# Kernel optimization log

Measured on AMD Instinct MI355X. Metric: run time of the kernel, lower is better.

The kernel has to match this reference:

```python
import jax, jax.numpy as jnp
import numpy as np

NX, NY = 1024, 512
LX, LY = 0.26, 0.12
NU = 1e-4
U_INLET = 0.1
DX = LX / (NX - 1)
DY = LY / (NY - 1)
W_CONT, W_MOM, W_BC = 1.0, 0.1, 1.0


def _pad_x(f):
    # replicate pad along x axis (dim -2)
    return jnp.pad(f, ((0, 0), (0, 0), (1, 1), (0, 0)), mode='edge')


def _pad_y(f):
    return jnp.pad(f, ((0, 0), (0, 0), (0, 0), (1, 1)), mode='edge')


def ddx(f):
    p = _pad_x(f)
    return (p[:, :, 2:, :] - p[:, :, :-2, :]) / (2.0 * DX)


def ddy(f):
    p = _pad_y(f)
    return (p[:, :, :, 2:] - p[:, :, :, :-2]) / (2.0 * DY)


def d2dx2(f):
    p = _pad_x(f)
    return (p[:, :, 2:, :] - 2.0 * f + p[:, :, :-2, :]) / (DX * DX)


def d2dy2(f):
    p = _pad_y(f)
    return (p[:, :, :, 2:] - 2.0 * f + p[:, :, :, :-2]) / (DY * DY)


def masked_mean(x, mask):
    return (x * mask).sum() / jnp.maximum(mask.sum(), 1.0)


def region_masks(x_in):
    r = x_in[:, 1:2].astype(jnp.float32)  # [B,1,NX,NY] region codes
    fluid = (r > 0.5).astype(jnp.float32)
    obstacle = (r < 0.5).astype(jnp.float32)
    wall = ((r > 1.5) & (r < 2.5)).astype(jnp.float32)
    inlet = ((r > 2.5) & (r < 3.5)).astype(jnp.float32)
    outlet = (r > 3.5).astype(jnp.float32)
    noslip = ((obstacle + wall) > 0.5).astype(jnp.float32)
    # interior = fluid with zeroed 1-cell border
    border = jnp.zeros((NX, NY), jnp.float32).at[1:-1, 1:-1].set(1.0)
    interior = fluid * border
    return fluid, interior, noslip, inlet, outlet


def setup_inputs() -> dict:
    key = jax.random.key(0)
    k1, k2 = jax.random.split(key)
    y_hat = jax.random.normal(k1, (16, 3, NX, NY), dtype=jnp.float32)
    x_in = jax.random.randint(k2, (16, 2, NX, NY), 0, 5).astype(jnp.int32)
    return {'y_hat': y_hat, 'x_in': x_in}


def reference(y_hat, x_in):
    ux = y_hat[:, 0:1]
    uy = y_hat[:, 1:2]
    p = y_hat[:, 2:3]
    fluid, interior, noslip, inlet, outlet = region_masks(x_in)

    # continuity
    div = ddx(ux) + ddy(uy)
    l_cont = masked_mean(div ** 2, interior)

    # momentum
    res_x = ux * ddx(ux) + uy * ddy(ux) + ddx(p) - NU * (d2dx2(ux) + d2dy2(ux))
    res_y = ux * ddx(uy) + uy * ddy(uy) + ddy(p) - NU * (d2dx2(uy) + d2dy2(uy))
    l_mom = masked_mean(res_x ** 2, interior) + masked_mean(res_y ** 2, interior)

    # boundary (masked_mean already returns 0 for empty masks via denom clamp)
    l_bc = masked_mean(ux ** 2, noslip) + masked_mean(uy ** 2, noslip)
    l_bc = l_bc + masked_mean((ux - U_INLET) ** 2, inlet) + masked_mean(uy ** 2, inlet)
    l_bc = l_bc + masked_mean(ddx(ux) ** 2, outlet)

    total = W_CONT * l_cont + W_MOM * l_mom + W_BC * l_bc
    return jnp.stack([l_cont, l_mom, l_bc, total])
```

## Files before the change

### kernel.cpp

```cpp
#include <hip/hip_runtime.h>


namespace {
constexpr int NXc  = 1024;
constexpr int NYc  = 512;
constexpr int NXYc = NXc * NYc;
constexpr int NBc  = 16;
constexpr int NTHR = 512;
constexpr int NACC = 10;
constexpr int TR   = 8;
constexpr int NCH  = NXc / TR;
constexpr int NBLK = NBc * NCH;
constexpr int NXCD = 8;
constexpr int QX   = NBLK / NXCD;
}

__global__ __launch_bounds__(NTHR) void pil_main(const float* __restrict__ y,
                                                 const int* __restrict__ xin,
                                                 float* __restrict__ partial) {
  constexpr double DXd = 0.26 / 1023.0;
  constexpr double DYd = 0.12 / 511.0;
  const float INV2DX = (float)(1.0 / (2.0 * DXd));
  const float INV2DY = (float)(1.0 / (2.0 * DYd));
  const float INVDX2 = (float)(1.0 / (DXd * DXd));
  const float INVDY2 = (float)(1.0 / (DYd * DYd));
  constexpr float NU = 1e-4f;
  constexpr float U_INLET = 0.1f;

  __shared__ float lf[3][TR + 2][NYc];

  const int l   = threadIdx.x & 63;
  const int w   = threadIdx.x >> 6;
  const int swz = (blockIdx.x % NXCD) * QX + blockIdx.x / NXCD;
  const int b   = swz >> 7;
  const int i0  = (swz & (NCH - 1)) * TR;

  const float* __restrict__ ux = y + (size_t)b * 3 * NXYc;
  const float* __restrict__ uy = ux + NXYc;
  const float* __restrict__ pp = ux + 2 * NXYc;
  const int*   __restrict__ rp = xin + (size_t)(2 * b + 1) * NXYc;

  for (int c = w; c < 60; c += 8) {
    const int f  = c / 20;
    const int cc = c % 20;
    const int rw = cc >> 1;
    const int h  = cc & 1;
    int gi = i0 - 1 + rw;
    gi = gi < 0 ? 0 : (gi > NXc - 1 ? NXc - 1 : gi);
    const float* base = (f == 0) ? ux : ((f == 1) ? uy : pp);
    const float* g = base + gi * NYc + h * 256 + l * 4;
    float* d = &lf[f][rw][h * 256];
    __builtin_amdgcn_global_load_lds(
        (const __attribute__((address_space(1))) void*)g,
        (__attribute__((address_space(3))) void*)d, 16, 0, 0);
  }

  const int i = i0 + w;
  const int4 R0 = *reinterpret_cast<const int4*>(rp + i * NYc + (l << 2));
  const int4 R1 = *reinterpret_cast<const int4*>(rp + i * NYc + 256 + (l << 2));

  __syncthreads();

  float a[NACC];
#pragma unroll
  for (int k = 0; k < NACC; ++k) a[k] = 0.f;

  const bool irow = (i >= 1) & (i <= NXc - 2);

#pragma unroll
  for (int h = 0; h < 2; ++h) {
    const int j0 = h * 256 + (l << 2);

    const float4 Cx = *reinterpret_cast<const float4*>(&lf[0][w + 1][j0]);
    const float4 Cy = *reinterpret_cast<const float4*>(&lf[1][w + 1][j0]);
    const float4 Cp = *reinterpret_cast<const float4*>(&lf[2][w + 1][j0]);
    const float4 Px = *reinterpret_cast<const float4*>(&lf[0][w][j0]);
    const float4 Py = *reinterpret_cast<const float4*>(&lf[1][w][j0]);
    const float4 Pp = *reinterpret_cast<const float4*>(&lf[2][w][j0]);
    const float4 Nx = *reinterpret_cast<const float4*>(&lf[0][w + 2][j0]);
    const float4 Ny = *reinterpret_cast<const float4*>(&lf[1][w + 2][j0]);
    const float4 Np = *reinterpret_cast<const float4*>(&lf[2][w + 2][j0]);
    const int4   R4 = h ? R1 : R0;

    const int jm = (j0 == 0) ? 0 : j0 - 1;
    const int jp = (j0 + 4 > NYc - 1) ? NYc - 1 : j0 + 4;
    const float lx = lf[0][w + 1][jm], rx = lf[0][w + 1][jp];
    const float ly = lf[1][w + 1][jm], ry = lf[1][w + 1][jp];
    const float lq = lf[2][w + 1][jm], rq = lf[2][w + 1][jp];

    const float cx[6]  = {lx, Cx.x, Cx.y, Cx.z, Cx.w, rx};
    const float cy_[6] = {ly, Cy.x, Cy.y, Cy.z, Cy.w, ry};
    const float cp_[6] = {lq, Cp.x, Cp.y, Cp.z, Cp.w, rq};
    const float pxA[4] = {Px.x, Px.y, Px.z, Px.w};
    const float pyA[4] = {Py.x, Py.y, Py.z, Py.w};
    const float ppA[4] = {Pp.x, Pp.y, Pp.z, Pp.w};
    const float nxA[4] = {Nx.x, Nx.y, Nx.z, Nx.w};
    const float nyA[4] = {Ny.x, Ny.y, Ny.z, Ny.w};
    const float npA[4] = {Np.x, Np.y, Np.z, Np.w};
    const int   rA[4]  = {R4.x, R4.y, R4.z, R4.w};

#pragma unroll
    for (int e = 0; e < 4; ++e) {
      const int   rg   = rA[e];
      const float c_ux = cx[e + 1], c_uy = cy_[e + 1];
      const float uxm = cx[e],      uxp = cx[e + 2];
      const float uym = cy_[e],     uyp = cy_[e + 2];
      const float pm_ = cp_[e],     pq_ = cp_[e + 2];

      const float ddx_ux = (nxA[e] - pxA[e]) * INV2DX;
      const float ddy_ux = (uxp - uxm) * INV2DY;
      const float ddx_uy = (nyA[e] - pyA[e]) * INV2DX;
      const float ddy_uy = (uyp - uym) * INV2DY;

      const int j = j0 + e;
      const bool jedge = (j == 0) | (j == NYc - 1);
      const bool interior = (rg >= 1) & irow & (!jedge);
      if (interior) {
        const float dv    = ddx_ux + ddy_uy;
        const float d2xux = (nxA[e] - 2.f * c_ux + pxA[e]) * INVDX2;
        const float d2yux = (uxp - 2.f * c_ux + uxm) * INVDY2;
        const float d2xuy = (nyA[e] - 2.f * c_uy + pyA[e]) * INVDX2;
        const float d2yuy = (uyp - 2.f * c_uy + uym) * INVDY2;
        const float ddx_p = (npA[e] - ppA[e]) * INV2DX;
        const float ddy_p = (pq_ - pm_) * INV2DY;
        const float rxv = c_ux * ddx_ux + c_uy * ddy_ux + ddx_p - NU * (d2xux + d2yux);
        const float ryv = c_ux * ddx_uy + c_uy * ddy_uy + ddy_p - NU * (d2xuy + d2yuy);
        a[0] += dv * dv;
        a[1] += rxv * rxv;
        a[2] += ryv * ryv;
        a[3] += 1.f;
      }
      if ((rg == 0) | (rg == 2)) {
        a[4] += c_ux * c_ux + c_uy * c_uy;
        a[5] += 1.f;
      }
      if (rg == 3) {
        const float d = c_ux - U_INLET;
        a[6] += d * d + c_uy * c_uy;
        a[7] += 1.f;
      }
      if (rg == 4) {
        a[8] += ddx_ux * ddx_ux;
        a[9] += 1.f;
      }
    }
  }

#pragma unroll
  for (int k = 0; k < NACC; ++k) {
    float v = a[k];
#pragma unroll
    for (int off = 32; off > 0; off >>= 1) v += __shfl_down(v, off, 64);
    a[k] = v;
  }

  __shared__ float sacc[NTHR / 64][NACC];
  if (l == 0) {
#pragma unroll
    for (int k = 0; k < NACC; ++k) sacc[w][k] = a[k];
  }
  __syncthreads();
  if (threadIdx.x < NACC) {
    float s = 0.f;
#pragma unroll
    for (int ww = 0; ww < NTHR / 64; ++ww) s += sacc[ww][threadIdx.x];
    partial[threadIdx.x * NBLK + blockIdx.x] = s;
  }
}

__global__ __launch_bounds__(256) void pil_finalize(const float* __restrict__ partial,
                                                    float* __restrict__ out) {
  __shared__ double sw[NACC][4];
  const int t = threadIdx.x;
  const int lane = t & 63, wave = t >> 6;
#pragma unroll
  for (int k = 0; k < NACC; ++k) {
    double v = 0.0;
    const float4* p4 = reinterpret_cast<const float4*>(partial + (size_t)k * NBLK);
    for (int bb = t; bb < NBLK / 4; bb += 256) {
      const float4 q = p4[bb];
      v += (double)q.x + (double)q.y + (double)q.z + (double)q.w;
    }
#pragma unroll
    for (int off = 32; off > 0; off >>= 1) v += __shfl_down(v, off, 64);
    if (lane == 0) sw[k][wave] = v;
  }
  __syncthreads();
  if (t == 0) {
    double acc[NACC];
#pragma unroll
    for (int k = 0; k < NACC; ++k) {
      double s = 0.0;
#pragma unroll
      for (int ww = 0; ww < 4; ++ww) s += sw[k][ww];
      acc[k] = s;
    }
    const double l_cont = acc[0] / fmax(acc[3], 1.0);
    const double l_mom  = (acc[1] + acc[2]) / fmax(acc[3], 1.0);
    const double l_bc   = acc[4] / fmax(acc[5], 1.0)
                        + acc[6] / fmax(acc[7], 1.0)
                        + acc[8] / fmax(acc[9], 1.0);
    const double total  = 1.0 * l_cont + 0.1 * l_mom + 1.0 * l_bc;
    out[0] = (float)l_cont;
    out[1] = (float)l_mom;
    out[2] = (float)l_bc;
    out[3] = (float)total;
  }
}

extern "C" void kernel_launch(void* const* d_in, const int* in_sizes, int n_in,
                              void* d_out, int out_size, void* d_ws, size_t ws_size,
                              hipStream_t stream) {
  const float* y   = (const float*)d_in[0];
  const int*   xin = (const int*)d_in[1];
  float* partial   = (float*)d_ws;

  pil_main<<<NBLK, NTHR, 0, stream>>>(y, xin, partial);
  pil_finalize<<<1, 256, 0, stream>>>(partial, (float*)d_out);
}
```

Measured before the change: 47.16 us.

## Make blocks persistent over eight row tiles with double-buffered async LDS staging

Each block now processes eight consecutive 8-row tiles instead of one, giving 256 blocks in total. The next tile's halo rows are staged into a second LDS buffer with global_load_lds while the current tile is computed, using manual vmcnt waits and barriers. This amortizes launch cost and overlaps memory with compute. In exchange it needs 120 KB of dynamic LDS per block, which cuts occupancy to one block per CU, and it relies on hand-counted vmcnt values. The finalize kernel now reads one partial per thread since there are only 256 partials.

```diff
diff --git a/kernel.cpp b/kernel.cpp
--- a/kernel.cpp
+++ b/kernel.cpp
@@ -9,15 +9,18 @@
 constexpr int NTHR = 512;
 constexpr int NACC = 10;
 constexpr int TR   = 8;
-constexpr int NCH  = NXc / TR;
-constexpr int NBLK = NBc * NCH;
+constexpr int TPB  = 8;
+constexpr int NBLK = NBc * NXc / (TR * TPB);
 constexpr int NXCD = 8;
 constexpr int QX   = NBLK / NXCD;
+constexpr int BUFE = 3 * (TR + 2) * NYc;
 }
 
 __global__ __launch_bounds__(NTHR) void pil_main(const float* __restrict__ y,
                                                  const int* __restrict__ xin,
                                                  float* __restrict__ partial) {
+  extern __shared__ float lds[];
+
   constexpr double DXd = 0.26 / 1023.0;
   constexpr double DYd = 0.12 / 511.0;
   const float INV2DX = (float)(1.0 / (2.0 * DXd));
@@ -27,123 +30,152 @@
   constexpr float NU = 1e-4f;
   constexpr float U_INLET = 0.1f;
 
-  __shared__ float lf[3][TR + 2][NYc];
-
   const int l   = threadIdx.x & 63;
   const int w   = threadIdx.x >> 6;
   const int swz = (blockIdx.x % NXCD) * QX + blockIdx.x / NXCD;
-  const int b   = swz >> 7;
-  const int i0  = (swz & (NCH - 1)) * TR;
+  const int b   = swz >> 4;
+  const int sub = swz & 15;
+  const int bi0 = sub * (TR * TPB);
 
   const float* __restrict__ ux = y + (size_t)b * 3 * NXYc;
   const float* __restrict__ uy = ux + NXYc;
   const float* __restrict__ pp = ux + 2 * NXYc;
   const int*   __restrict__ rp = xin + (size_t)(2 * b + 1) * NXYc;
 
-  for (int c = w; c < 60; c += 8) {
-    const int f  = c / 20;
-    const int cc = c % 20;
-    const int rw = cc >> 1;
-    const int h  = cc & 1;
-    int gi = i0 - 1 + rw;
-    gi = gi < 0 ? 0 : (gi > NXc - 1 ? NXc - 1 : gi);
-    const float* base = (f == 0) ? ux : ((f == 1) ? uy : pp);
-    const float* g = base + gi * NYc + h * 256 + l * 4;
-    float* d = &lf[f][rw][h * 256];
-    __builtin_amdgcn_global_load_lds(
-        (const __attribute__((address_space(1))) void*)g,
-        (__attribute__((address_space(3))) void*)d, 16, 0, 0);
-  }
-
-  const int i = i0 + w;
-  const int4 R0 = *reinterpret_cast<const int4*>(rp + i * NYc + (l << 2));
-  const int4 R1 = *reinterpret_cast<const int4*>(rp + i * NYc + 256 + (l << 2));
-
-  __syncthreads();
+  auto stage = [&](int t, int q) {
+    const int ti0 = bi0 + t * TR;
+#pragma unroll
+    for (int k = 0; k < 8; ++k) {
+      const int c = k * 8 + w;
+      if (c < 60) {
+        const int f  = c / 20;
+        const int cc = c % 20;
+        const int rw = cc >> 1;
+        const int h  = cc & 1;
+        int gi = ti0 - 1 + rw;
+        gi = gi < 0 ? 0 : (gi > NXc - 1 ? NXc - 1 : gi);
+        const float* base = (f == 0) ? ux : ((f == 1) ? uy : pp);
+        const float* g = base + gi * NYc + h * 256 + l * 4;
+        float* d = lds + q * BUFE + f * ((TR + 2) * NYc) + rw * NYc + h * 256;
+        __builtin_amdgcn_global_load_lds(
+            (const __attribute__((address_space(1))) void*)g,
+            (__attribute__((address_space(3))) void*)d, 16, 0, 0);
+      }
+    }
+  };
 
   float a[NACC];
 #pragma unroll
   for (int k = 0; k < NACC; ++k) a[k] = 0.f;
 
-  const bool irow = (i >= 1) & (i <= NXc - 2);
-
-#pragma unroll
-  for (int h = 0; h < 2; ++h) {
-    const int j0 = h * 256 + (l << 2);
-
-    const float4 Cx = *reinterpret_cast<const float4*>(&lf[0][w + 1][j0]);
-    const float4 Cy = *reinterpret_cast<const float4*>(&lf[1][w + 1][j0]);
-    const float4 Cp = *reinterpret_cast<const float4*>(&lf[2][w + 1][j0]);
-    const float4 Px = *reinterpret_cast<const float4*>(&lf[0][w][j0]);
-    const float4 Py = *reinterpret_cast<const float4*>(&lf[1][w][j0]);
-    const float4 Pp = *reinterpret_cast<const float4*>(&lf[2][w][j0]);
-    const float4 Nx = *reinterpret_cast<const float4*>(&lf[0][w + 2][j0]);
-    const float4 Ny = *reinterpret_cast<const float4*>(&lf[1][w + 2][j0]);
-    const float4 Np = *reinterpret_cast<const float4*>(&lf[2][w + 2][j0]);
-    const int4   R4 = h ? R1 : R0;
-
-    const int jm = (j0 == 0) ? 0 : j0 - 1;
-    const int jp = (j0 + 4 > NYc - 1) ? NYc - 1 : j0 + 4;
-    const float lx = lf[0][w + 1][jm], rx = lf[0][w + 1][jp];
-    const float ly = lf[1][w + 1][jm], ry = lf[1][w + 1][jp];
-    const float lq = lf[2][w + 1][jm], rq = lf[2][w + 1][jp];
-
-    const float cx[6]  = {lx, Cx.x, Cx.y, Cx.z, Cx.w, rx};
-    const float cy_[6] = {ly, Cy.x, Cy.y, Cy.z, Cy.w, ry};
-    const float cp_[6] = {lq, Cp.x, Cp.y, Cp.z, Cp.w, rq};
-    const float pxA[4] = {Px.x, Px.y, Px.z, Px.w};
-    const float pyA[4] = {Py.x, Py.y, Py.z, Py.w};
-    const float ppA[4] = {Pp.x, Pp.y, Pp.z, Pp.w};
-    const float nxA[4] = {Nx.x, Nx.y, Nx.z, Nx.w};
-    const float nyA[4] = {Ny.x, Ny.y, Ny.z, Ny.w};
-    const float npA[4] = {Np.x, Np.y, Np.z, Np.w};
-    const int   rA[4]  = {R4.x, R4.y, R4.z, R4.w};
-
-#pragma unroll
-    for (int e = 0; e < 4; ++e) {
-      const int   rg   = rA[e];
-      const float c_ux = cx[e + 1], c_uy = cy_[e + 1];
-      const float uxm = cx[e],      uxp = cx[e + 2];
-      const float uym = cy_[e],     uyp = cy_[e + 2];
-      const float pm_ = cp_[e],     pq_ = cp_[e + 2];
-
-      const float ddx_ux = (nxA[e] - pxA[e]) * INV2DX;
-      const float ddy_ux = (uxp - uxm) * INV2DY;
-      const float ddx_uy = (nyA[e] - pyA[e]) * INV2DX;
-      const float ddy_uy = (uyp - uym) * INV2DY;
-
-      const int j = j0 + e;
-      const bool jedge = (j == 0) | (j == NYc - 1);
-      const bool interior = (rg >= 1) & irow & (!jedge);
-      if (interior) {
-        const float dv    = ddx_ux + ddy_uy;
-        const float d2xux = (nxA[e] - 2.f * c_ux + pxA[e]) * INVDX2;
-        const float d2yux = (uxp - 2.f * c_ux + uxm) * INVDY2;
-        const float d2xuy = (nyA[e] - 2.f * c_uy + pyA[e]) * INVDX2;
-        const float d2yuy = (uyp - 2.f * c_uy + uym) * INVDY2;
-        const float ddx_p = (npA[e] - ppA[e]) * INV2DX;
-        const float ddy_p = (pq_ - pm_) * INV2DY;
-        const float rxv = c_ux * ddx_ux + c_uy * ddy_ux + ddx_p - NU * (d2xux + d2yux);
-        const float ryv = c_ux * ddx_uy + c_uy * ddy_uy + ddy_p - NU * (d2xuy + d2yuy);
-        a[0] += dv * dv;
-        a[1] += rxv * rxv;
-        a[2] += ryv * ryv;
-        a[3] += 1.f;
+  stage(0, 0);
+
+#pragma unroll 2
+  for (int t = 0; t < TPB; ++t) {
+    const int q = t & 1;
+    const int i = bi0 + t * TR + w;
+
+    const int4 R0 = *reinterpret_cast<const int4*>(rp + i * NYc + (l << 2));
+    const int4 R1 = *reinterpret_cast<const int4*>(rp + i * NYc + 256 + (l << 2));
+    asm volatile("" ::: "memory");
+
+    if (t + 1 < TPB) {
+      stage(t + 1, q ^ 1);
+      if (w < 4) asm volatile("s_waitcnt vmcnt(8)" ::: "memory");
+      else       asm volatile("s_waitcnt vmcnt(7)" ::: "memory");
+    } else {
+      asm volatile("s_waitcnt vmcnt(0)" ::: "memory");
+    }
+    __builtin_amdgcn_s_barrier();
+    asm volatile("" ::: "memory");
+
+    const float* Lf = lds + q * BUFE;
+#define LF(f, row, col) Lf[(f) * ((TR + 2) * NYc) + (row) * NYc + (col)]
+
+    const bool irow = (i >= 1) & (i <= NXc - 2);
+
+#pragma unroll
+    for (int h = 0; h < 2; ++h) {
+      const int j0 = h * 256 + (l << 2);
+
+      const float4 Cx = *reinterpret_cast<const float4*>(&LF(0, w + 1, j0));
+      const float4 Cy = *reinterpret_cast<const float4*>(&LF(1, w + 1, j0));
+      const float4 Cp = *reinterpret_cast<const float4*>(&LF(2, w + 1, j0));
+      const float4 Px = *reinterpret_cast<const float4*>(&LF(0, w, j0));
+      const float4 Py = *reinterpret_cast<const float4*>(&LF(1, w, j0));
+      const float4 Pp = *reinterpret_cast<const float4*>(&LF(2, w, j0));
+      const float4 Nx = *reinterpret_cast<const float4*>(&LF(0, w + 2, j0));
+      const float4 Ny = *reinterpret_cast<const float4*>(&LF(1, w + 2, j0));
+      const float4 Np = *reinterpret_cast<const float4*>(&LF(2, w + 2, j0));
+      const int4   R4 = h ? R1 : R0;
+
+      const int jm = (j0 == 0) ? 0 : j0 - 1;
+      const int jp = (j0 + 4 > NYc - 1) ? NYc - 1 : j0 + 4;
+      const float lx = LF(0, w + 1, jm), rx = LF(0, w + 1, jp);
+      const float ly = LF(1, w + 1, jm), ry = LF(1, w + 1, jp);
+      const float lq = LF(2, w + 1, jm), rq = LF(2, w + 1, jp);
+
+      const float cx[6]  = {lx, Cx.x, Cx.y, Cx.z, Cx.w, rx};
+      const float cy_[6] = {ly, Cy.x, Cy.y, Cy.z, Cy.w, ry};
+      const float cp_[6] = {lq, Cp.x, Cp.y, Cp.z, Cp.w, rq};
+      const float pxA[4] = {Px.x, Px.y, Px.z, Px.w};
+      const float pyA[4] = {Py.x, Py.y, Py.z, Py.w};
+      const float ppA[4] = {Pp.x, Pp.y, Pp.z, Pp.w};
+      const float nxA[4] = {Nx.x, Nx.y, Nx.z, Nx.w};
+      const float nyA[4] = {Ny.x, Ny.y, Ny.z, Ny.w};
+      const float npA[4] = {Np.x, Np.y, Np.z, Np.w};
+      const int   rA[4]  = {R4.x, R4.y, R4.z, R4.w};
+
+#pragma unroll
+      for (int e = 0; e < 4; ++e) {
+        const int   rg   = rA[e];
+        const float c_ux = cx[e + 1], c_uy = cy_[e + 1];
+        const float uxm = cx[e],      uxp = cx[e + 2];
+        const float uym = cy_[e],     uyp = cy_[e + 2];
+        const float pm_ = cp_[e],     pq_ = cp_[e + 2];
+
+        const float ddx_ux = (nxA[e] - pxA[e]) * INV2DX;
+        const float ddy_ux = (uxp - uxm) * INV2DY;
+        const float ddx_uy = (nyA[e] - pyA[e]) * INV2DX;
+        const float ddy_uy = (uyp - uym) * INV2DY;
+
+        const int j = j0 + e;
+        const bool jedge = (j == 0) | (j == NYc - 1);
+        const bool interior = (rg >= 1) & irow & (!jedge);
+        if (interior) {
+          const float dv    = ddx_ux + ddy_uy;
+          const float d2xux = (nxA[e] - 2.f * c_ux + pxA[e]) * INVDX2;
+          const float d2yux = (uxp - 2.f * c_ux + uxm) * INVDY2;
+          const float d2xuy = (nyA[e] - 2.f * c_uy + pyA[e]) * INVDX2;
+          const float d2yuy = (uyp - 2.f * c_uy + uym) * INVDY2;
+          const float ddx_p = (npA[e] - ppA[e]) * INV2DX;
+          const float ddy_p = (pq_ - pm_) * INV2DY;
+          const float rxv = c_ux * ddx_ux + c_uy * ddy_ux + ddx_p - NU * (d2xux + d2yux);
+          const float ryv = c_ux * ddx_uy + c_uy * ddy_uy + ddy_p - NU * (d2xuy + d2yuy);
+          a[0] += dv * dv;
+          a[1] += rxv * rxv;
+          a[2] += ryv * ryv;
+          a[3] += 1.f;
+        }
+        if ((rg == 0) | (rg == 2)) {
+          a[4] += c_ux * c_ux + c_uy * c_uy;
+          a[5] += 1.f;
+        }
+        if (rg == 3) {
+          const float d = c_ux - U_INLET;
+          a[6] += d * d + c_uy * c_uy;
+          a[7] += 1.f;
+        }
+        if (rg == 4) {
+          a[8] += ddx_ux * ddx_ux;
+          a[9] += 1.f;
+        }
       }
-      if ((rg == 0) | (rg == 2)) {
-        a[4] += c_ux * c_ux + c_uy * c_uy;
-        a[5] += 1.f;
-      }
-      if (rg == 3) {
-        const float d = c_ux - U_INLET;
-        a[6] += d * d + c_uy * c_uy;
-        a[7] += 1.f;
-      }
-      if (rg == 4) {
-        a[8] += ddx_ux * ddx_ux;
-        a[9] += 1.f;
-      }
-    }
+    }
+#undef LF
+
+    asm volatile("" ::: "memory");
+    __builtin_amdgcn_s_barrier();
   }
 
 #pragma unroll
@@ -154,16 +186,16 @@
     a[k] = v;
   }
 
-  __shared__ float sacc[NTHR / 64][NACC];
+  float* sacc = lds;
   if (l == 0) {
 #pragma unroll
-    for (int k = 0; k < NACC; ++k) sacc[w][k] = a[k];
+    for (int k = 0; k < NACC; ++k) sacc[w * NACC + k] = a[k];
   }
   __syncthreads();
   if (threadIdx.x < NACC) {
     float s = 0.f;
 #pragma unroll
-    for (int ww = 0; ww < NTHR / 64; ++ww) s += sacc[ww][threadIdx.x];
+    for (int ww = 0; ww < NTHR / 64; ++ww) s += sacc[ww * NACC + threadIdx.x];
     partial[threadIdx.x * NBLK + blockIdx.x] = s;
   }
 }
@@ -175,12 +207,7 @@
   const int lane = t & 63, wave = t >> 6;
 #pragma unroll
   for (int k = 0; k < NACC; ++k) {
-    double v = 0.0;
-    const float4* p4 = reinterpret_cast<const float4*>(partial + (size_t)k * NBLK);
-    for (int bb = t; bb < NBLK / 4; bb += 256) {
-      const float4 q = p4[bb];
-      v += (double)q.x + (double)q.y + (double)q.z + (double)q.w;
-    }
+    double v = (double)partial[k * NBLK + t];
 #pragma unroll
     for (int off = 32; off > 0; off >>= 1) v += __shfl_down(v, off, 64);
     if (lane == 0) sw[k][wave] = v;
@@ -215,6 +242,7 @@
   const int*   xin = (const int*)d_in[1];
   float* partial   = (float*)d_ws;
 
-  pil_main<<<NBLK, NTHR, 0, stream>>>(y, xin, partial);
+  const size_t dyn_lds = 2 * (size_t)BUFE * sizeof(float);
+  pil_main<<<NBLK, NTHR, dyn_lds, stream>>>(y, xin, partial);
   pil_finalize<<<1, 256, 0, stream>>>(partial, (float*)d_out);
 }
```

Measured after the change: 88.89 us. +88.5%, slower.

## Halve row tile and block size, give each lane 8 contiguous columns with shuffle halos

Applied to the files above, without the earlier changes.

Blocks shrink from 512 to 256 threads and from 8 to 4 rows, doubling the block count and halving the shared tile. Each lane now handles 8 contiguous columns and gets its left and right neighbours through wavefront shuffles instead of extra scalar LDS reads. The staging loop is fully unrolled at 9 iterations. More blocks mean more halo rows re-read from global memory and more partial sums for the finalize kernel to reduce.

```diff
diff --git a/kernel.cpp b/kernel.cpp
--- a/kernel.cpp
+++ b/kernel.cpp
@@ -6,9 +6,9 @@
 constexpr int NYc  = 512;
 constexpr int NXYc = NXc * NYc;
 constexpr int NBc  = 16;
-constexpr int NTHR = 512;
+constexpr int NTHR = 256;
 constexpr int NACC = 10;
-constexpr int TR   = 8;
+constexpr int TR   = 4;
 constexpr int NCH  = NXc / TR;
 constexpr int NBLK = NBc * NCH;
 constexpr int NXCD = 8;
@@ -32,7 +32,7 @@
   const int l   = threadIdx.x & 63;
   const int w   = threadIdx.x >> 6;
   const int swz = (blockIdx.x % NXCD) * QX + blockIdx.x / NXCD;
-  const int b   = swz >> 7;
+  const int b   = swz >> 8;
   const int i0  = (swz & (NCH - 1)) * TR;
 
   const float* __restrict__ ux = y + (size_t)b * 3 * NXYc;
@@ -40,9 +40,11 @@
   const float* __restrict__ pp = ux + 2 * NXYc;
   const int*   __restrict__ rp = xin + (size_t)(2 * b + 1) * NXYc;
 
-  for (int c = w; c < 60; c += 8) {
-    const int f  = c / 20;
-    const int cc = c % 20;
+#pragma unroll
+  for (int k = 0; k < 9; ++k) {
+    const int c  = k * 4 + w;
+    const int f  = c / 12;
+    const int cc = c % 12;
     const int rw = cc >> 1;
     const int h  = cc & 1;
     int gi = i0 - 1 + rw;
@@ -56,93 +58,100 @@
   }
 
   const int i = i0 + w;
-  const int4 R0 = *reinterpret_cast<const int4*>(rp + i * NYc + (l << 2));
-  const int4 R1 = *reinterpret_cast<const int4*>(rp + i * NYc + 256 + (l << 2));
+  const int jc = l << 3;
+  const int4 R0 = *reinterpret_cast<const int4*>(rp + i * NYc + jc);
+  const int4 R1 = *reinterpret_cast<const int4*>(rp + i * NYc + jc + 4);
 
   __syncthreads();
 
+  const float4 Cxl = *reinterpret_cast<const float4*>(&lf[0][w + 1][jc]);
+  const float4 Cxh = *reinterpret_cast<const float4*>(&lf[0][w + 1][jc + 4]);
+  const float4 Cyl = *reinterpret_cast<const float4*>(&lf[1][w + 1][jc]);
+  const float4 Cyh = *reinterpret_cast<const float4*>(&lf[1][w + 1][jc + 4]);
+  const float4 Cpl = *reinterpret_cast<const float4*>(&lf[2][w + 1][jc]);
+  const float4 Cph = *reinterpret_cast<const float4*>(&lf[2][w + 1][jc + 4]);
+  const float4 Pxl = *reinterpret_cast<const float4*>(&lf[0][w][jc]);
+  const float4 Pxh = *reinterpret_cast<const float4*>(&lf[0][w][jc + 4]);
+  const float4 Pyl = *reinterpret_cast<const float4*>(&lf[1][w][jc]);
+  const float4 Pyh = *reinterpret_cast<const float4*>(&lf[1][w][jc + 4]);
+  const float4 Ppl = *reinterpret_cast<const float4*>(&lf[2][w][jc]);
+  const float4 Pph = *reinterpret_cast<const float4*>(&lf[2][w][jc + 4]);
+  const float4 Nxl = *reinterpret_cast<const float4*>(&lf[0][w + 2][jc]);
+  const float4 Nxh = *reinterpret_cast<const float4*>(&lf[0][w + 2][jc + 4]);
+  const float4 Nyl = *reinterpret_cast<const float4*>(&lf[1][w + 2][jc]);
+  const float4 Nyh = *reinterpret_cast<const float4*>(&lf[1][w + 2][jc + 4]);
+  const float4 Npl = *reinterpret_cast<const float4*>(&lf[2][w + 2][jc]);
+  const float4 Nph = *reinterpret_cast<const float4*>(&lf[2][w + 2][jc + 4]);
+
   float a[NACC];
 #pragma unroll
   for (int k = 0; k < NACC; ++k) a[k] = 0.f;
 
+  const float cx[8]  = {Cxl.x, Cxl.y, Cxl.z, Cxl.w, Cxh.x, Cxh.y, Cxh.z, Cxh.w};
+  const float cy_[8] = {Cyl.x, Cyl.y, Cyl.z, Cyl.w, Cyh.x, Cyh.y, Cyh.z, Cyh.w};
+  const float cp_[8] = {Cpl.x, Cpl.y, Cpl.z, Cpl.w, Cph.x, Cph.y, Cph.z, Cph.w};
+  const float pxA[8] = {Pxl.x, Pxl.y, Pxl.z, Pxl.w, Pxh.x, Pxh.y, Pxh.z, Pxh.w};
+  const float pyA[8] = {Pyl.x, Pyl.y, Pyl.z, Pyl.w, Pyh.x, Pyh.y, Pyh.z, Pyh.w};
+  const float ppA[8] = {Ppl.x, Ppl.y, Ppl.z, Ppl.w, Pph.x, Pph.y, Pph.z, Pph.w};
+  const float nxA[8] = {Nxl.x, Nxl.y, Nxl.z, Nxl.w, Nxh.x, Nxh.y, Nxh.z, Nxh.w};
+  const float nyA[8] = {Nyl.x, Nyl.y, Nyl.z, Nyl.w, Nyh.x, Nyh.y, Nyh.z, Nyh.w};
+  const float npA[8] = {Npl.x, Npl.y, Npl.z, Npl.w, Nph.x, Nph.y, Nph.z, Nph.w};
+  const int   rA[8]  = {R0.x, R0.y, R0.z, R0.w, R1.x, R1.y, R1.z, R1.w};
+
+  float lxx = __shfl_up(cx[7], 1, 64);    if (l == 0)  lxx = cx[0];
+  float rxx = __shfl_down(cx[0], 1, 64);  if (l == 63) rxx = cx[7];
+  float lyy = __shfl_up(cy_[7], 1, 64);   if (l == 0)  lyy = cy_[0];
+  float ryy = __shfl_down(cy_[0], 1, 64); if (l == 63) ryy = cy_[7];
+  float lpp = __shfl_up(cp_[7], 1, 64);   if (l == 0)  lpp = cp_[0];
+  float rpp = __shfl_down(cp_[0], 1, 64); if (l == 63) rpp = cp_[7];
+
   const bool irow = (i >= 1) & (i <= NXc - 2);
 
 #pragma unroll
-  for (int h = 0; h < 2; ++h) {
-    const int j0 = h * 256 + (l << 2);
-
-    const float4 Cx = *reinterpret_cast<const float4*>(&lf[0][w + 1][j0]);
-    const float4 Cy = *reinterpret_cast<const float4*>(&lf[1][w + 1][j0]);
-    const float4 Cp = *reinterpret_cast<const float4*>(&lf[2][w + 1][j0]);
-    const float4 Px = *reinterpret_cast<const float4*>(&lf[0][w][j0]);
-    const float4 Py = *reinterpret_cast<const float4*>(&lf[1][w][j0]);
-    const float4 Pp = *reinterpret_cast<const float4*>(&lf[2][w][j0]);
-    const float4 Nx = *reinterpret_cast<const float4*>(&lf[0][w + 2][j0]);
-    const float4 Ny = *reinterpret_cast<const float4*>(&lf[1][w + 2][j0]);
-    const float4 Np = *reinterpret_cast<const float4*>(&lf[2][w + 2][j0]);
-    const int4   R4 = h ? R1 : R0;
-
-    const int jm = (j0 == 0) ? 0 : j0 - 1;
-    const int jp = (j0 + 4 > NYc - 1) ? NYc - 1 : j0 + 4;
-    const float lx = lf[0][w + 1][jm], rx = lf[0][w + 1][jp];
-    const float ly = lf[1][w + 1][jm], ry = lf[1][w + 1][jp];
-    const float lq = lf[2][w + 1][jm], rq = lf[2][w + 1][jp];
-
-    const float cx[6]  = {lx, Cx.x, Cx.y, Cx.z, Cx.w, rx};
-    const float cy_[6] = {ly, Cy.x, Cy.y, Cy.z, Cy.w, ry};
-    const float cp_[6] = {lq, Cp.x, Cp.y, Cp.z, Cp.w, rq};
-    const float pxA[4] = {Px.x, Px.y, Px.z, Px.w};
-    const float pyA[4] = {Py.x, Py.y, Py.z, Py.w};
-    const float ppA[4] = {Pp.x, Pp.y, Pp.z, Pp.w};
-    const float nxA[4] = {Nx.x, Nx.y, Nx.z, Nx.w};
-    const float nyA[4] = {Ny.x, Ny.y, Ny.z, Ny.w};
-    const float npA[4] = {Np.x, Np.y, Np.z, Np.w};
-    const int   rA[4]  = {R4.x, R4.y, R4.z, R4.w};
-
-#pragma unroll
-    for (int e = 0; e < 4; ++e) {
-      const int   rg   = rA[e];
-      const float c_ux = cx[e + 1], c_uy = cy_[e + 1];
-      const float uxm = cx[e],      uxp = cx[e + 2];
-      const float uym = cy_[e],     uyp = cy_[e + 2];
-      const float pm_ = cp_[e],     pq_ = cp_[e + 2];
-
-      const float ddx_ux = (nxA[e] - pxA[e]) * INV2DX;
-      const float ddy_ux = (uxp - uxm) * INV2DY;
-      const float ddx_uy = (nyA[e] - pyA[e]) * INV2DX;
-      const float ddy_uy = (uyp - uym) * INV2DY;
-
-      const int j = j0 + e;
-      const bool jedge = (j == 0) | (j == NYc - 1);
-      const bool interior = (rg >= 1) & irow & (!jedge);
-      if (interior) {
-        const float dv    = ddx_ux + ddy_uy;
-        const float d2xux = (nxA[e] - 2.f * c_ux + pxA[e]) * INVDX2;
-        const float d2yux = (uxp - 2.f * c_ux + uxm) * INVDY2;
-        const float d2xuy = (nyA[e] - 2.f * c_uy + pyA[e]) * INVDX2;
-        const float d2yuy = (uyp - 2.f * c_uy + uym) * INVDY2;
-        const float ddx_p = (npA[e] - ppA[e]) * INV2DX;
-        const float ddy_p = (pq_ - pm_) * INV2DY;
-        const float rxv = c_ux * ddx_ux + c_uy * ddy_ux + ddx_p - NU * (d2xux + d2yux);
-        const float ryv = c_ux * ddx_uy + c_uy * ddy_uy + ddy_p - NU * (d2xuy + d2yuy);
-        a[0] += dv * dv;
-        a[1] += rxv * rxv;
-        a[2] += ryv * ryv;
-        a[3] += 1.f;
-      }
-      if ((rg == 0) | (rg == 2)) {
-        a[4] += c_ux * c_ux + c_uy * c_uy;
-        a[5] += 1.f;
-      }
-      if (rg == 3) {
-        const float d = c_ux - U_INLET;
-        a[6] += d * d + c_uy * c_uy;
-        a[7] += 1.f;
-      }
-      if (rg == 4) {
-        a[8] += ddx_ux * ddx_ux;
-        a[9] += 1.f;
-      }
+  for (int e = 0; e < 8; ++e) {
+    const int   r    = rA[e];
+    const float c_ux = cx[e], c_uy = cy_[e];
+    const float uxm = (e == 0) ? lxx : cx[e - 1];
+    const float uxp = (e == 7) ? rxx : cx[e + 1];
+    const float uym = (e == 0) ? lyy : cy_[e - 1];
+    const float uyp = (e == 7) ? ryy : cy_[e + 1];
+    const float pm_ = (e == 0) ? lpp : cp_[e - 1];
+    const float pq_ = (e == 7) ? rpp : cp_[e + 1];
+
+    const float ddx_ux = (nxA[e] - pxA[e]) * INV2DX;
+    const float ddy_ux = (uxp - uxm) * INV2DY;
+    const float ddx_uy = (nyA[e] - pyA[e]) * INV2DX;
+    const float ddy_uy = (uyp - uym) * INV2DY;
+
+    const bool jedge = ((l == 0) & (e == 0)) | ((l == 63) & (e == 7));
+    const bool interior = (r >= 1) & irow & (!jedge);
+    if (interior) {
+      const float dv    = ddx_ux + ddy_uy;
+      const float d2xux = (nxA[e] - 2.f * c_ux + pxA[e]) * INVDX2;
+      const float d2yux = (uxp - 2.f * c_ux + uxm) * INVDY2;
+      const float d2xuy = (nyA[e] - 2.f * c_uy + pyA[e]) * INVDX2;
+      const float d2yuy = (uyp - 2.f * c_uy + uym) * INVDY2;
+      const float ddx_p = (npA[e] - ppA[e]) * INV2DX;
+      const float ddy_p = (pq_ - pm_) * INV2DY;
+      const float rxv = c_ux * ddx_ux + c_uy * ddy_ux + ddx_p - NU * (d2xux + d2yux);
+      const float ryv = c_ux * ddx_uy + c_uy * ddy_uy + ddy_p - NU * (d2xuy + d2yuy);
+      a[0] += dv * dv;
+      a[1] += rxv * rxv;
+      a[2] += ryv * ryv;
+      a[3] += 1.f;
+    }
+    if ((r == 0) | (r == 2)) {
+      a[4] += c_ux * c_ux + c_uy * c_uy;
+      a[5] += 1.f;
+    }
+    if (r == 3) {
+      const float d = c_ux - U_INLET;
+      a[6] += d * d + c_uy * c_uy;
+      a[7] += 1.f;
+    }
+    if (r == 4) {
+      a[8] += ddx_ux * ddx_ux;
+      a[9] += 1.f;
     }
   }
 
```

New measurement: 53.50 us. 1.13x slower.
